# Optimization experiments

Hardware: AMD Instinct MI355X
Metric: run time of the kernel (lower is better)

The kernel has to match this reference:

```python
import jax, jax.numpy as jnp
import numpy as np

N = 65536
INPUT_DIM = 768
OUTPUT_DIM = 256
NUM_LEVELS = 4
CODEBOOK_SIZE = 1024
BETA = 0.25
LN_EPS = 1e-5


def setup_inputs() -> dict:
    key = jax.random.key(0)
    ks = jax.random.split(key, 12)
    s_in = 1.0 / np.sqrt(INPUT_DIM)
    s_out = 1.0 / np.sqrt(OUTPUT_DIM)
    return {
        "x": jax.random.normal(ks[0], (N, INPUT_DIM), dtype=jnp.float32),
        "ln_g": jnp.ones((INPUT_DIM,), dtype=jnp.float32),
        "ln_b": jnp.zeros((INPUT_DIM,), dtype=jnp.float32),
        # weights stored [in, out] (torch Linear is [out, in]); math identical
        "W1": jax.random.uniform(ks[1], (INPUT_DIM, OUTPUT_DIM), jnp.float32, -s_in, s_in),
        "b1": jax.random.uniform(ks[2], (OUTPUT_DIM,), jnp.float32, -s_in, s_in),
        "W2": jax.random.uniform(ks[3], (OUTPUT_DIM, OUTPUT_DIM), jnp.float32, -s_out, s_out),
        "b2": jax.random.uniform(ks[4], (OUTPUT_DIM,), jnp.float32, -s_out, s_out),
        "Wd1": jax.random.uniform(ks[5], (OUTPUT_DIM, INPUT_DIM), jnp.float32, -s_out, s_out),
        "bd1": jax.random.uniform(ks[6], (INPUT_DIM,), jnp.float32, -s_out, s_out),
        "Wd2": jax.random.uniform(ks[7], (INPUT_DIM, INPUT_DIM), jnp.float32, -s_in, s_in),
        "bd2": jax.random.uniform(ks[8], (INPUT_DIM,), jnp.float32, -s_in, s_in),
        "codebooks": jax.random.normal(ks[9], (NUM_LEVELS, CODEBOOK_SIZE, OUTPUT_DIM), dtype=jnp.float32),
    }


def _quantize_with_loss(enc, codebooks):
    residual = enc
    q_final = jnp.zeros_like(enc)
    commit = jnp.float32(0.0)
    indices = []
    for l in range(NUM_LEVELS):
        cb = codebooks[l]  # [K, D]
        # squared euclidean distance: ||r||^2 - 2 r.c + ||c||^2 -> [N, K]
        d = (jnp.sum(residual ** 2, axis=1, keepdims=True)
             - 2.0 * residual @ cb.T
             + jnp.sum(cb ** 2, axis=1)[None, :])
        idx = jnp.argmin(d, axis=1)  # [N]
        indices.append(idx)
        q = cb[idx]  # [N, D]
        commit = commit + jnp.mean((jax.lax.stop_gradient(residual) - q) ** 2)
        q_final = q_final + q
        q_st = residual + jax.lax.stop_gradient(q - residual)  # straight-through
        residual = residual - q_st
    return q_final, jnp.stack(indices, axis=1), commit


def reference(x, ln_g, ln_b, W1, b1, W2, b2, Wd1, bd1, Wd2, bd2, codebooks):
    # encoder: LayerNorm -> Linear -> ReLU -> Linear
    mu = jnp.mean(x, axis=-1, keepdims=True)
    var = jnp.mean((x - mu) ** 2, axis=-1, keepdims=True)
    xn = (x - mu) * jax.lax.rsqrt(var + LN_EPS) * ln_g + ln_b
    enc = jax.nn.relu(xn @ W1 + b1) @ W2 + b2  # [N, D]

    q, indices, commit = _quantize_with_loss(enc, codebooks)

    # decoder: Linear -> ReLU -> Linear
    recon = jax.nn.relu(q @ Wd1 + bd1) @ Wd2 + bd2  # [N, input_dim]

    rec_loss = jnp.mean((recon - x) ** 2)
    loss = rec_loss + BETA * commit
    return loss, recon, indices
```

## Files before the change

### kernel.cpp

```cpp
#include <hip/hip_runtime.h>
#include <hip/hip_bf16.h>
#include <stdint.h>

#define NROWS 65536
#define INDIM 768
#define ODIM  256
#define NLEV  4
#define CBS   1024
#define TAUQ  2e-2f

typedef __attribute__((ext_vector_type(8))) short short8;
typedef __attribute__((ext_vector_type(4))) float f32x4;

__device__ __forceinline__ float bf2f(unsigned short u) {
    union { unsigned int i; float f; } v; v.i = ((unsigned int)u) << 16; return v.f;
}
__device__ __forceinline__ unsigned short f2bf(float f) {
    union { float f; unsigned int i; } v; v.f = f;
    unsigned int r = v.i + 0x7fffu + ((v.i >> 16) & 1u);
    return (unsigned short)(r >> 16);
}
__device__ __forceinline__ f32x4 mfma_bf16(short8 a, short8 b, f32x4 c) {
    return __builtin_amdgcn_mfma_f32_16x16x32_bf16(a, b, c, 0, 0, 0);
}

typedef const __attribute__((address_space(1))) unsigned int GUI;
typedef __attribute__((address_space(3))) unsigned int LUI;
__device__ __forceinline__ void gld16(const void* g, void* l) {
    __builtin_amdgcn_global_load_lds((GUI*)g, (LUI*)l, 16, 0, 0);
}

__global__ void k_init(double* __restrict__ acc) {
    if (threadIdx.x < 2) acc[threadIdx.x] = 0.0;
}

__global__ __launch_bounds__(64) void k_cnorm(const float* __restrict__ cb, float* __restrict__ cn) {
    const int code = blockIdx.x;
    const float* r = cb + (size_t)code * ODIM + threadIdx.x * 4;
    float4 v = *(const float4*)r;
    float s = fmaf(v.x, v.x, fmaf(v.y, v.y, fmaf(v.z, v.z, v.w * v.w)));
    #pragma unroll
    for (int o = 32; o > 0; o >>= 1) s += __shfl_xor(s, o);
    if (threadIdx.x == 0) cn[code] = s;
}

__global__ __launch_bounds__(256) void k_split(const float* __restrict__ cb,
                                               unsigned short* __restrict__ ch,
                                               unsigned short* __restrict__ cl) {
    const size_t i = ((size_t)blockIdx.x * 256 + threadIdx.x) * 4;
    float4 v = *(const float4*)(cb + i);
    float e[4] = {v.x, v.y, v.z, v.w};
    ushort4 h, l;
    unsigned short* hp = &h.x; unsigned short* lp = &l.x;
    #pragma unroll
    for (int j = 0; j < 4; ++j) {
        unsigned short hh = f2bf(e[j]);
        hp[j] = hh;
        lp[j] = f2bf(e[j] - bf2f(hh));
    }
    *(ushort4*)(ch + i) = h;
    *(ushort4*)(cl + i) = l;
}

__global__ __launch_bounds__(256) void k_cbt(const float* __restrict__ cb, float* __restrict__ ct) {
    __shared__ float T[32][33];
    const int l  = blockIdx.z;
    const int c0 = blockIdx.x << 5;
    const int k0 = blockIdx.y << 5;
    const int tx = threadIdx.x & 31, ty = threadIdx.x >> 5;
    const float* src = cb + ((size_t)l * CBS + c0) * ODIM + k0;
    #pragma unroll
    for (int i = 0; i < 4; ++i)
        T[ty + (i << 3)][tx] = src[(size_t)(ty + (i << 3)) * ODIM + tx];
    __syncthreads();
    float* dst = ct + ((size_t)l * ODIM + k0) * CBS + c0;
    #pragma unroll
    for (int i = 0; i < 4; ++i)
        dst[(size_t)(ty + (i << 3)) * CBS + tx] = T[tx][ty + (i << 3)];
}

__global__ __launch_bounds__(256) void k_wt(const float* __restrict__ W,
                                            unsigned short* __restrict__ Th,
                                            unsigned short* __restrict__ Tl,
                                            const int K, const int N, const int split) {
    const int n = blockIdx.x;
    for (int k = threadIdx.x; k < K; k += 256) {
        float v = W[(size_t)k * N + n];
        unsigned short h = f2bf(v);
        Th[(size_t)n * K + k] = h;
        if (split) Tl[(size_t)n * K + k] = f2bf(v - bf2f(h));
    }
}

__global__ __launch_bounds__(256) void k_ln(const float* __restrict__ x,
                                            float* __restrict__ mu, float* __restrict__ rsig) {
    const int row = blockIdx.x;
    const int t = threadIdx.x;
    const float* xr = x + (size_t)row * INDIM;
    float a = xr[t], b = xr[t + 256], c = xr[t + 512];
    float s1 = a + b + c;
    float s2 = fmaf(a, a, fmaf(b, b, c * c));
    #pragma unroll
    for (int o = 32; o > 0; o >>= 1) { s1 += __shfl_xor(s1, o); s2 += __shfl_xor(s2, o); }
    __shared__ float r1[4], r2[4];
    if ((t & 63) == 0) { r1[t >> 6] = s1; r2[t >> 6] = s2; }
    __syncthreads();
    if (t == 0) {
        float S1 = (r1[0] + r1[1]) + (r1[2] + r1[3]);
        float S2 = (r2[0] + r2[1]) + (r2[2] + r2[3]);
        float m = S1 * (1.0f / INDIM);
        float var = S2 * (1.0f / INDIM) - m * m;
        mu[row] = m;
        rsig[row] = rsqrtf(var + 1e-5f);
    }
}

template <int AMODE, int SPLIT, int EPI>
__global__ __launch_bounds__(256, 2) void k_gemm_mfma(
    const void* __restrict__ Ap, const unsigned short* __restrict__ Bh,
    const unsigned short* __restrict__ Bl,
    const float* __restrict__ bias, void* __restrict__ Cp,
    const int K, const int Nc,
    const float* __restrict__ mu, const float* __restrict__ rsig,
    const float* __restrict__ lng, const float* __restrict__ lnb,
    const float* __restrict__ xref, double* __restrict__ acc_rec)
{
    __shared__ __align__(16) unsigned short BhS[256][40];
    __shared__ __align__(16) unsigned short BlS[SPLIT ? 256 : 8][SPLIT ? 40 : 8];
    __shared__ float credsh[4];

    const int t = threadIdx.x;
    const int wave = t >> 6, lane = t & 63;
    const int lg = lane >> 4, lm = lane & 15;
    const int wm = wave >> 1, wn = wave & 1;
    const size_t rowb = (size_t)blockIdx.y * 128 + wm * 64;
    const int nb = blockIdx.x << 8;

    f32x4 acc[4][8];
    #pragma unroll
    for (int mt = 0; mt < 4; ++mt)
        #pragma unroll
        for (int nt = 0; nt < 8; ++nt) acc[mt][nt] = (f32x4){0.f, 0.f, 0.f, 0.f};

    float lnm[4], lnr[4];
    if (AMODE == 1) {
        #pragma unroll
        for (int mt = 0; mt < 4; ++mt) {
            lnm[mt] = mu[rowb + (mt << 4) + lm];
            lnr[mt] = rsig[rowb + (mt << 4) + lm];
        }
    }

    for (int kk = 0; kk < K; kk += 32) {
        short8 Ah[4], Al[4];
        if (AMODE == 2) {
            #pragma unroll
            for (int mt = 0; mt < 4; ++mt)
                Ah[mt] = *(const short8*)((const unsigned short*)Ap +
                          (rowb + (mt << 4) + lm) * (size_t)K + kk + (lg << 3));
        } else {
            float g[8], bb[8];
            if (AMODE == 1) {
                float4 g0 = *(const float4*)(lng + kk + (lg << 3));
                float4 g1 = *(const float4*)(lng + kk + (lg << 3) + 4);
                float4 b0 = *(const float4*)(lnb + kk + (lg << 3));
                float4 b1 = *(const float4*)(lnb + kk + (lg << 3) + 4);
                g[0]=g0.x; g[1]=g0.y; g[2]=g0.z; g[3]=g0.w; g[4]=g1.x; g[5]=g1.y; g[6]=g1.z; g[7]=g1.w;
                bb[0]=b0.x; bb[1]=b0.y; bb[2]=b0.z; bb[3]=b0.w; bb[4]=b1.x; bb[5]=b1.y; bb[6]=b1.z; bb[7]=b1.w;
            }
            #pragma unroll
            for (int mt = 0; mt < 4; ++mt) {
                const float* ar = (const float*)Ap + (rowb + (mt << 4) + lm) * (size_t)K + kk + (lg << 3);
                float4 a0 = *(const float4*)ar;
                float4 a1 = *(const float4*)(ar + 4);
                float e[8] = {a0.x, a0.y, a0.z, a0.w, a1.x, a1.y, a1.z, a1.w};
                #pragma unroll
                for (int j = 0; j < 8; ++j) {
                    float v = e[j];
                    if (AMODE == 1) v = fmaf((v - lnm[mt]) * lnr[mt], g[j], bb[j]);
                    unsigned short h = f2bf(v);
                    Ah[mt][j] = (short)h;
                    Al[mt][j] = (short)f2bf(v - bf2f(h));
                }
            }
        }
        __syncthreads();
        {
            const unsigned short* gh = Bh + (size_t)nb * K + kk;
            #pragma unroll
            for (int it = 0; it < 4; ++it) {
                const int idx = (it << 8) + t;
                const int n = idx >> 2, sl = idx & 3;
                *(uint4*)&BhS[n][sl << 3] = *(const uint4*)(gh + (size_t)n * K + (sl << 3));
            }
            if (SPLIT) {
                const unsigned short* gl = Bl + (size_t)nb * K + kk;
                #pragma unroll
                for (int it = 0; it < 4; ++it) {
                    const int idx = (it << 8) + t;
                    const int n = idx >> 2, sl = idx & 3;
                    *(uint4*)&BlS[n][sl << 3] = *(const uint4*)(gl + (size_t)n * K + (sl << 3));
                }
            }
        }
        __syncthreads();
        #pragma unroll
        for (int nt = 0; nt < 8; ++nt) {
            const int nl = (wn << 7) + (nt << 4) + lm;
            short8 bh = *(const short8*)&BhS[nl][lg << 3];
            if (!SPLIT) {
                #pragma unroll
                for (int mt = 0; mt < 4; ++mt)
                    acc[mt][nt] = mfma_bf16(Ah[mt], bh, acc[mt][nt]);
            } else {
                short8 bl = *(const short8*)&BlS[nl][lg << 3];
                #pragma unroll
                for (int mt = 0; mt < 4; ++mt) {
                    acc[mt][nt] = mfma_bf16(Ah[mt], bh, acc[mt][nt]);
                    acc[mt][nt] = mfma_bf16(Al[mt], bh, acc[mt][nt]);
                    acc[mt][nt] = mfma_bf16(Ah[mt], bl, acc[mt][nt]);
                }
            }
        }
    }

    float lsum = 0.0f;
    #pragma unroll
    for (int nt = 0; nt < 8; ++nt) {
        const int col = nb + (wn << 7) + (nt << 4) + lm;
        const float bs = bias[col];
        #pragma unroll
        for (int mt = 0; mt < 4; ++mt) {
            #pragma unroll
            for (int r = 0; r < 4; ++r) {
                float v = acc[mt][nt][r] + bs;
                if (EPI == 0 || EPI == 2) v = fmaxf(v, 0.0f);
                const size_t row = rowb + (mt << 4) + (lg << 2) + r;
                if (EPI == 2) {
                    ((unsigned short*)Cp)[row * Nc + col] = f2bf(v);
                } else {
                    ((float*)Cp)[row * Nc + col] = v;
                }
                if (EPI == 3) {
                    const float d = v - xref[row * Nc + col];
                    lsum = fmaf(d, d, lsum);
                }
            }
        }
    }
    if (EPI == 3) {
        #pragma unroll
        for (int o = 32; o > 0; o >>= 1) lsum += __shfl_xor(lsum, o);
        if (lane == 0) credsh[wave] = lsum;
        __syncthreads();
        if (t == 0) atomicAdd(acc_rec, (double)((credsh[0] + credsh[1]) + (credsh[2] + credsh[3])));
    }
}

__global__ __launch_bounds__(256, 2) void k_quant_mfma(
    const float* __restrict__ enc, const float* __restrict__ cb,
    const unsigned short* __restrict__ cbh, const unsigned short* __restrict__ cbl,
    const float* __restrict__ cnorm, unsigned short* __restrict__ qf, float* __restrict__ oidx,
    int* __restrict__ flag, double* __restrict__ acc_commit)
{
    __shared__ __align__(128) unsigned short Bh[2][32][256];
    __shared__ __align__(128) unsigned short Bl[2][32][256];
    __shared__ __align__(16) int rowidxsh[128];
    __shared__ float credsh[4];

    const int t = threadIdx.x;
    const int wave = t >> 6, lane = t & 63;
    const int lg = lane >> 4, lm = lane & 15;
    const size_t rowbase = (size_t)blockIdx.x * 128 + wave * 32;

#define STAGE_CHUNK(b_, gh_, gl_) do {                                          \
    _Pragma("unroll")                                                           \
    for (int i_ = 0; i_ < 4; ++i_) {                                            \
        const int seg_ = (i_ << 2) + wave;                                      \
        const int off_ = (seg_ << 10) + (lane << 4);                            \
        const int src_ = off_ ^ (((off_ >> 9) & 7) << 4);                       \
        gld16((const char*)(gh_) + src_, (char*)&Bh[b_][0][0] + (seg_ << 10));  \
        gld16((const char*)(gl_) + src_, (char*)&Bl[b_][0][0] + (seg_ << 10));  \
    }                                                                           \
} while (0)

    STAGE_CHUNK(0, cbh, cbl);
    int buf = 0;

    short8 Ah[2][8], Al[2][8];
    #pragma unroll
    for (int mt = 0; mt < 2; ++mt)
        #pragma unroll
        for (int s = 0; s < 8; ++s) {
            const float* er = enc + (rowbase + mt * 16 + lm) * ODIM + s * 32 + lg * 8;
            float4 e0 = *(const float4*)er;
            float4 e1 = *(const float4*)(er + 4);
            float e[8] = {e0.x, e0.y, e0.z, e0.w, e1.x, e1.y, e1.z, e1.w};
            #pragma unroll
            for (int j = 0; j < 8; ++j) {
                unsigned short h = f2bf(e[j]);
                Ah[mt][s][j] = (short)h;
                Al[mt][s][j] = (short)f2bf(e[j] - bf2f(h));
            }
        }

    float commit_local = 0.0f;
    int flg[2][4] = {{0, 0, 0, 0}, {0, 0, 0, 0}};

    for (int l = 0; l < NLEV; ++l) {
        float bestv[2][4], b2v[2][4];
        int besti[2][4];
        #pragma unroll
        for (int mt = 0; mt < 2; ++mt)
            #pragma unroll
            for (int r = 0; r < 4; ++r) { bestv[mt][r] = 3.4e38f; b2v[mt][r] = 3.4e38f; besti[mt][r] = 0; }

        for (int ch = 0; ch < 32; ++ch) {
            __syncthreads();
            {
                const int cc = (l << 5) + ch + 1;
                if (cc < 128) {
                    const unsigned short* gh = cbh + ((size_t)(cc >> 5) << 18) + ((size_t)(cc & 31) << 13);
                    const unsigned short* gl = cbl + ((size_t)(cc >> 5) << 18) + ((size_t)(cc & 31) << 13);
                    STAGE_CHUNK(buf ^ 1, gh, gl);
                }
            }
            const int cbase = ch << 5;
            const unsigned short* bbh = &Bh[buf][0][0];
            const unsigned short* bbl = &Bl[buf][0][0];
            #pragma unroll
            for (int nt = 0; nt < 2; ++nt) {
                const int rowB = (nt << 4) + lm;
                const int rbase = rowB << 9;
                const int xm = (rowB & 7) << 4;
                f32x4 p0[2], p1[2];
                #pragma unroll
                for (int mt = 0; mt < 2; ++mt) {
                    p0[mt] = (f32x4){0.f, 0.f, 0.f, 0.f};
                    p1[mt] = (f32x4){0.f, 0.f, 0.f, 0.f};
                }
                #pragma unroll
                for (int s = 0; s < 8; ++s) {
                    const int a = rbase + (((s << 6) + (lg << 4)) ^ xm);
                    short8 bh = *(const short8*)((const char*)bbh + a);
                    short8 bl = *(const short8*)((const char*)bbl + a);
                    p0[0] = mfma_bf16(Ah[0][s], bh, p0[0]);
                    p0[1] = mfma_bf16(Ah[1][s], bh, p0[1]);
                    p1[0] = mfma_bf16(Al[0][s], bh, p1[0]);
                    p1[1] = mfma_bf16(Al[1][s], bh, p1[1]);
                    p1[0] = mfma_bf16(Ah[0][s], bl, p1[0]);
                    p1[1] = mfma_bf16(Ah[1][s], bl, p1[1]);
                }
                const int code = cbase + (nt << 4) + lm;
                const float cn = cnorm[(l << 10) + code];
                #pragma unroll
                for (int mt = 0; mt < 2; ++mt)
                    #pragma unroll
                    for (int r = 0; r < 4; ++r) {
                        const float d = fmaf(-2.0f, p0[mt][r] + p1[mt][r], cn);
                        if (d < bestv[mt][r]) {
                            b2v[mt][r] = bestv[mt][r]; bestv[mt][r] = d; besti[mt][r] = code;
                        } else {
                            b2v[mt][r] = fminf(b2v[mt][r], d);
                        }
                    }
            }
            buf ^= 1;
        }

        #pragma unroll
        for (int mt = 0; mt < 2; ++mt) {
            int iv[4];
            #pragma unroll
            for (int r = 0; r < 4; ++r) {
                float bv = bestv[mt][r], b2 = b2v[mt][r];
                int bi = besti[mt][r];
                #pragma unroll
                for (int off = 1; off < 16; off <<= 1) {
                    float ov = __shfl_xor(bv, off);
                    float o2 = __shfl_xor(b2, off);
                    int   oi = __shfl_xor(bi, off);
                    if (ov < bv)      { b2 = fminf(bv, o2); bv = ov; bi = oi; }
                    else if (ov > bv) { b2 = fminf(b2, ov); }
                    else              { b2 = bv; bi = (oi < bi) ? oi : bi; }
                }
                flg[mt][r] |= (b2 - bv < TAUQ) ? 1 : 0;
                iv[r] = bi;
                if (lm == 0)
                    oidx[(rowbase + (mt << 4) + (lg << 2) + r) * NLEV + l] = (float)bi;
            }
            if (lm == 0)
                *(int4*)&rowidxsh[(wave << 5) + (mt << 4) + (lg << 2)] = make_int4(iv[0], iv[1], iv[2], iv[3]);
        }
        __syncthreads();

        const size_t lbase = (size_t)l * CBS * ODIM;
        #pragma unroll
        for (int mt = 0; mt < 2; ++mt) {
            const int ci = rowidxsh[(wave << 5) + (mt << 4) + lm];
            const float* cr = cb + lbase + (size_t)ci * ODIM + lg * 8;
            #pragma unroll
            for (int s = 0; s < 8; ++s) {
                float4 c0 = *(const float4*)(cr + (s << 5));
                float4 c1 = *(const float4*)(cr + (s << 5) + 4);
                float c[8] = {c0.x, c0.y, c0.z, c0.w, c1.x, c1.y, c1.z, c1.w};
                #pragma unroll
                for (int j = 0; j < 8; ++j) {
                    float rr = bf2f((unsigned short)Ah[mt][s][j]) + bf2f((unsigned short)Al[mt][s][j]) - c[j];
                    commit_local = fmaf(rr, rr, commit_local);
                    unsigned short h = f2bf(rr);
                    Ah[mt][s][j] = (short)h;
                    Al[mt][s][j] = (short)f2bf(rr - bf2f(h));
                }
            }
        }
    }
#undef STAGE_CHUNK

    #pragma unroll
    for (int mt = 0; mt < 2; ++mt)
        #pragma unroll
        for (int s = 0; s < 8; ++s) {
            const size_t ro = (rowbase + mt * 16 + lm) * ODIM + s * 32 + lg * 8;
            float4 e0 = *(const float4*)(enc + ro);
            float4 e1 = *(const float4*)(enc + ro + 4);
            float e[8] = {e0.x, e0.y, e0.z, e0.w, e1.x, e1.y, e1.z, e1.w};
            unsigned short q[8];
            #pragma unroll
            for (int j = 0; j < 8; ++j)
                q[j] = f2bf(e[j] - (bf2f((unsigned short)Ah[mt][s][j]) + bf2f((unsigned short)Al[mt][s][j])));
            *(ushort4*)(qf + ro)     = make_ushort4(q[0], q[1], q[2], q[3]);
            *(ushort4*)(qf + ro + 4) = make_ushort4(q[4], q[5], q[6], q[7]);
        }

    if (lm == 0) {
        #pragma unroll
        for (int mt = 0; mt < 2; ++mt)
            #pragma unroll
            for (int r = 0; r < 4; ++r)
                flag[rowbase + (mt << 4) + (lg << 2) + r] = flg[mt][r];
    }

    #pragma unroll
    for (int o = 32; o > 0; o >>= 1) commit_local += __shfl_xor(commit_local, o);
    if (lane == 0) credsh[wave] = commit_local;
    __syncthreads();
    if (t == 0) atomicAdd(acc_commit, (double)((credsh[0] + credsh[1]) + (credsh[2] + credsh[3])));
}

__global__ __launch_bounds__(256) void k_fix(
    const int* __restrict__ flag, const float* __restrict__ x,
    const float* __restrict__ lng, const float* __restrict__ lnb,
    const float* __restrict__ W1, const float* __restrict__ b1,
    const float* __restrict__ W2, const float* __restrict__ b2,
    const float* __restrict__ cb, const float* __restrict__ ct,
    float* __restrict__ oidx)
{
    const int row = blockIdx.x;
    if (!flag[row]) return;
    const int t = threadIdx.x;
    __shared__ double xn[INDIM];
    __shared__ double hs[ODIM];
    __shared__ double r[ODIM];
    __shared__ double rv_[4];
    __shared__ int ri_[4];
    __shared__ int selidx;

    const float* xr = x + (size_t)row * INDIM;
    double xa = (double)xr[t], xb = (double)xr[t + 256], xc = (double)xr[t + 512];
    double s1 = xa + xb + xc;
    double s2 = xa * xa + xb * xb + xc * xc;
    #pragma unroll
    for (int o = 32; o > 0; o >>= 1) { s1 += __shfl_xor(s1, o); s2 += __shfl_xor(s2, o); }
    __shared__ double w1r[4], w2r[4];
    if ((t & 63) == 0) { w1r[t >> 6] = s1; w2r[t >> 6] = s2; }
    __syncthreads();
    double S1 = (w1r[0] + w1r[1]) + (w1r[2] + w1r[3]);
    double S2 = (w2r[0] + w2r[1]) + (w2r[2] + w2r[3]);
    double mu = S1 / (double)INDIM;
    double var = S2 / (double)INDIM - mu * mu;
    double rs = 1.0 / sqrt(var + 1e-5);
    xn[t]       = (xa - mu) * rs * (double)lng[t]       + (double)lnb[t];
    xn[t + 256] = (xb - mu) * rs * (double)lng[t + 256] + (double)lnb[t + 256];
    xn[t + 512] = (xc - mu) * rs * (double)lng[t + 512] + (double)lnb[t + 512];
    __syncthreads();
    {
        double a0 = 0.0, a1 = 0.0, a2 = 0.0, a3 = 0.0;
        for (int k = 0; k < INDIM; k += 4) {
            a0 = fma(xn[k + 0], (double)W1[(size_t)(k + 0) * ODIM + t], a0);
            a1 = fma(xn[k + 1], (double)W1[(size_t)(k + 1) * ODIM + t], a1);
            a2 = fma(xn[k + 2], (double)W1[(size_t)(k + 2) * ODIM + t], a2);
            a3 = fma(xn[k + 3], (double)W1[(size_t)(k + 3) * ODIM + t], a3);
        }
        hs[t] = fmax(((a0 + a1) + (a2 + a3)) + (double)b1[t], 0.0);
    }
    __syncthreads();
    {
        double a0 = 0.0, a1 = 0.0, a2 = 0.0, a3 = 0.0;
        for (int k = 0; k < ODIM; k += 4) {
            a0 = fma(hs[k + 0], (double)W2[(size_t)(k + 0) * ODIM + t], a0);
            a1 = fma(hs[k + 1], (double)W2[(size_t)(k + 1) * ODIM + t], a1);
            a2 = fma(hs[k + 2], (double)W2[(size_t)(k + 2) * ODIM + t], a2);
            a3 = fma(hs[k + 3], (double)W2[(size_t)(k + 3) * ODIM + t], a3);
        }
        r[t] = ((a0 + a1) + (a2 + a3)) + (double)b2[t];
    }
    __syncthreads();

    for (int l = 0; l < NLEV; ++l) {
        const float* ctl = ct + (size_t)l * CBS * ODIM;
        double d0 = 0.0, d1 = 0.0, d2 = 0.0, d3 = 0.0;
        #pragma unroll 4
        for (int k = 0; k < ODIM; ++k) {
            const double rk = r[k];
            const float4 c4 = *(const float4*)(ctl + ((size_t)k << 10) + (t << 2));
            const double f0 = rk - (double)c4.x;
            const double f1 = rk - (double)c4.y;
            const double f2 = rk - (double)c4.z;
            const double f3 = rk - (double)c4.w;
            d0 = fma(f0, f0, d0); d1 = fma(f1, f1, d1);
            d2 = fma(f2, f2, d2); d3 = fma(f3, f3, d3);
        }
        double bv = d0; int bi = (t << 2);
        if (d1 < bv) { bv = d1; bi = (t << 2) + 1; }
        if (d2 < bv) { bv = d2; bi = (t << 2) + 2; }
        if (d3 < bv) { bv = d3; bi = (t << 2) + 3; }
        #pragma unroll
        for (int o = 32; o > 0; o >>= 1) {
            double ov = __shfl_xor(bv, o);
            int oi = __shfl_xor(bi, o);
            if (ov < bv || (ov == bv && oi < bi)) { bv = ov; bi = oi; }
        }
        if ((t & 63) == 0) { rv_[t >> 6] = bv; ri_[t >> 6] = bi; }
        __syncthreads();
        if (t == 0) {
            double fv = rv_[0]; int fi = ri_[0];
            #pragma unroll
            for (int w = 1; w < 4; ++w)
                if (rv_[w] < fv || (rv_[w] == fv && ri_[w] < fi)) { fv = rv_[w]; fi = ri_[w]; }
            selidx = fi;
            oidx[(size_t)row * NLEV + l] = (float)fi;
        }
        __syncthreads();
        r[t] = r[t] - (double)cb[(size_t)l * CBS * ODIM + (size_t)selidx * ODIM + t];
        __syncthreads();
    }
}

__global__ void k_fin(const double* __restrict__ acc, float* __restrict__ out) {
    if (threadIdx.x == 0)
        out[0] = (float)(acc[1] / ((double)NROWS * (double)INDIM) +
                         0.25 * (acc[0] / ((double)NROWS * (double)ODIM)));
}

extern "C" void kernel_launch(void* const* d_in, const int* in_sizes, int n_in,
                              void* d_out, int out_size, void* d_ws, size_t ws_size,
                              hipStream_t stream)
{
    const float* x   = (const float*)d_in[0];
    const float* lng = (const float*)d_in[1];
    const float* lnb = (const float*)d_in[2];
    const float* W1  = (const float*)d_in[3];
    const float* b1  = (const float*)d_in[4];
    const float* W2  = (const float*)d_in[5];
    const float* b2  = (const float*)d_in[6];
    const float* Wd1 = (const float*)d_in[7];
    const float* bd1 = (const float*)d_in[8];
    const float* Wd2 = (const float*)d_in[9];
    const float* bd2 = (const float*)d_in[10];
    const float* cbs = (const float*)d_in[11];

    char* ws = (char*)d_ws;
    const size_t MB = 1u << 20;
    const size_t O_ACC  = 0;
    const size_t O_CN   = 1024;
    const size_t O_MU   = O_CN + 16384;
    const size_t O_RS   = O_MU + (size_t)NROWS * 4;
    const size_t O_FLAG = O_RS + (size_t)NROWS * 4;
    const size_t O_ENC  = 1 * MB;
    const size_t O_QF   = 65 * MB;
    const size_t O_W1H  = 97 * MB;
    const size_t O_W1L  = O_W1H + (size_t)INDIM * ODIM * 2;
    const size_t O_W2H  = O_W1L + (size_t)INDIM * ODIM * 2;
    const size_t O_W2L  = O_W2H + (size_t)ODIM * ODIM * 2;
    const size_t O_WD1  = O_W2L + (size_t)ODIM * ODIM * 2;
    const size_t O_WD2  = O_WD1 + (size_t)ODIM * INDIM * 2;
    const size_t O_CBH  = 100 * MB;
    const size_t O_CBL  = 102 * MB;
    const size_t O_H1   = 104 * MB;
    const size_t O_CT   = O_H1;

    double* acc   = (double*)(ws + O_ACC);
    float* cnorm  = (float*)(ws + O_CN);
    float* mu     = (float*)(ws + O_MU);
    float* rsig   = (float*)(ws + O_RS);
    int*   flag   = (int*)(ws + O_FLAG);
    float* enc    = (float*)(ws + O_ENC);
    unsigned short* qf  = (unsigned short*)(ws + O_QF);
    unsigned short* w1h = (unsigned short*)(ws + O_W1H);
    unsigned short* w1l = (unsigned short*)(ws + O_W1L);
    unsigned short* w2h = (unsigned short*)(ws + O_W2H);
    unsigned short* w2l = (unsigned short*)(ws + O_W2L);
    unsigned short* wd1h = (unsigned short*)(ws + O_WD1);
    unsigned short* wd2h = (unsigned short*)(ws + O_WD2);
    unsigned short* cbh = (unsigned short*)(ws + O_CBH);
    unsigned short* cbl = (unsigned short*)(ws + O_CBL);
    float* h1     = (float*)(ws + O_H1);
    float* ct     = (float*)(ws + O_CT);
    unsigned short* hd = (unsigned short*)(ws + O_H1);

    float* outF  = (float*)d_out;
    float* recon = outF + 1;
    float* oidx  = outF + 1 + (size_t)NROWS * INDIM;

    k_init<<<1, 64, 0, stream>>>(acc);
    k_cnorm<<<NLEV * CBS, 64, 0, stream>>>(cbs, cnorm);
    k_ln<<<NROWS, 256, 0, stream>>>(x, mu, rsig);
    k_wt<<<ODIM, 256, 0, stream>>>(W1, w1h, w1l, INDIM, ODIM, 1);
    k_wt<<<ODIM, 256, 0, stream>>>(W2, w2h, w2l, ODIM, ODIM, 1);
    k_wt<<<INDIM, 256, 0, stream>>>(Wd1, wd1h, nullptr, ODIM, INDIM, 0);
    k_wt<<<INDIM, 256, 0, stream>>>(Wd2, wd2h, nullptr, INDIM, INDIM, 0);
    k_split<<<(NLEV * CBS * ODIM) / 1024, 256, 0, stream>>>(cbs, cbh, cbl);
    k_gemm_mfma<1, 1, 0><<<dim3(1, NROWS / 128), 256, 0, stream>>>(
        x, w1h, w1l, b1, h1, INDIM, ODIM, mu, rsig, lng, lnb, nullptr, nullptr);
    k_gemm_mfma<0, 1, 1><<<dim3(1, NROWS / 128), 256, 0, stream>>>(
        h1, w2h, w2l, b2, enc, ODIM, ODIM, nullptr, nullptr, nullptr, nullptr, nullptr, nullptr);
    k_cbt<<<dim3(32, 8, 4), 256, 0, stream>>>(cbs, ct);
    k_quant_mfma<<<NROWS / 128, 256, 0, stream>>>(enc, cbs, cbh, cbl, cnorm, qf, oidx, flag, acc);
    k_fix<<<NROWS, 256, 0, stream>>>(flag, x, lng, lnb, W1, b1, W2, b2, cbs, ct, oidx);
    k_gemm_mfma<2, 0, 2><<<dim3(INDIM / 256, NROWS / 128), 256, 0, stream>>>(
        qf, wd1h, nullptr, bd1, hd, ODIM, INDIM, nullptr, nullptr, nullptr, nullptr, nullptr, nullptr);
    k_gemm_mfma<2, 0, 3><<<dim3(INDIM / 256, NROWS / 128), 256, 0, stream>>>(
        hd, wd2h, nullptr, bd2, recon, INDIM, INDIM, nullptr, nullptr, nullptr, nullptr, x, acc + 1);
    k_fin<<<1, 64, 0, stream>>>(acc, outF);
}
```

Before: 1.626 ms.

## Shrink quantizer tile to 16 rows per wave with single-buffered padded LDS

Reworks the residual quantization kernel so each wave handles 16 rows instead of 32 and blocks cover 64 rows, doubling the grid and raising the occupancy target. The asynchronous double-buffered direct-to-LDS codebook staging with XOR swizzle is replaced by synchronous register-staged loads into a padded LDS tile, bracketed by two barriers per chunk. This aims to cut register pressure and raise occupancy, at the cost of halving codebook reuse per LDS load, doubling total codebook reads, and losing load/compute overlap.

```diff
diff --git a/kernel.cpp b/kernel.cpp
--- a/kernel.cpp
+++ b/kernel.cpp
@@ -22,12 +22,6 @@
 }
 __device__ __forceinline__ f32x4 mfma_bf16(short8 a, short8 b, f32x4 c) {
     return __builtin_amdgcn_mfma_f32_16x16x32_bf16(a, b, c, 0, 0, 0);
-}
-
-typedef const __attribute__((address_space(1))) unsigned int GUI;
-typedef __attribute__((address_space(3))) unsigned int LUI;
-__device__ __forceinline__ void gld16(const void* g, void* l) {
-    __builtin_amdgcn_global_load_lds((GUI*)g, (LUI*)l, 16, 0, 0);
 }
 
 __global__ void k_init(double* __restrict__ acc) {
@@ -257,124 +251,101 @@
     }
 }
 
-__global__ __launch_bounds__(256, 2) void k_quant_mfma(
+__global__ __launch_bounds__(256, 4) void k_quant_mfma(
     const float* __restrict__ enc, const float* __restrict__ cb,
     const unsigned short* __restrict__ cbh, const unsigned short* __restrict__ cbl,
     const float* __restrict__ cnorm, unsigned short* __restrict__ qf, float* __restrict__ oidx,
     int* __restrict__ flag, double* __restrict__ acc_commit)
 {
-    __shared__ __align__(128) unsigned short Bh[2][32][256];
-    __shared__ __align__(128) unsigned short Bl[2][32][256];
-    __shared__ __align__(16) int rowidxsh[128];
+    __shared__ __align__(16) unsigned short Bh[32][264];
+    __shared__ __align__(16) unsigned short Bl[32][264];
+    __shared__ __align__(16) int rowidxsh[64];
     __shared__ float credsh[4];
 
     const int t = threadIdx.x;
     const int wave = t >> 6, lane = t & 63;
     const int lg = lane >> 4, lm = lane & 15;
-    const size_t rowbase = (size_t)blockIdx.x * 128 + wave * 32;
-
-#define STAGE_CHUNK(b_, gh_, gl_) do {                                          \
-    _Pragma("unroll")                                                           \
-    for (int i_ = 0; i_ < 4; ++i_) {                                            \
-        const int seg_ = (i_ << 2) + wave;                                      \
-        const int off_ = (seg_ << 10) + (lane << 4);                            \
-        const int src_ = off_ ^ (((off_ >> 9) & 7) << 4);                       \
-        gld16((const char*)(gh_) + src_, (char*)&Bh[b_][0][0] + (seg_ << 10));  \
-        gld16((const char*)(gl_) + src_, (char*)&Bl[b_][0][0] + (seg_ << 10));  \
-    }                                                                           \
-} while (0)
-
-    STAGE_CHUNK(0, cbh, cbl);
-    int buf = 0;
-
-    short8 Ah[2][8], Al[2][8];
-    #pragma unroll
-    for (int mt = 0; mt < 2; ++mt)
-        #pragma unroll
-        for (int s = 0; s < 8; ++s) {
-            const float* er = enc + (rowbase + mt * 16 + lm) * ODIM + s * 32 + lg * 8;
-            float4 e0 = *(const float4*)er;
-            float4 e1 = *(const float4*)(er + 4);
-            float e[8] = {e0.x, e0.y, e0.z, e0.w, e1.x, e1.y, e1.z, e1.w};
-            #pragma unroll
-            for (int j = 0; j < 8; ++j) {
-                unsigned short h = f2bf(e[j]);
-                Ah[mt][s][j] = (short)h;
-                Al[mt][s][j] = (short)f2bf(e[j] - bf2f(h));
-            }
-        }
+    const size_t rowbase = (size_t)blockIdx.x * 64 + wave * 16;
+
+    short8 Ah[8], Al[8];
+    #pragma unroll
+    for (int s = 0; s < 8; ++s) {
+        const float* er = enc + (rowbase + lm) * ODIM + s * 32 + lg * 8;
+        float4 e0 = *(const float4*)er;
+        float4 e1 = *(const float4*)(er + 4);
+        float e[8] = {e0.x, e0.y, e0.z, e0.w, e1.x, e1.y, e1.z, e1.w};
+        #pragma unroll
+        for (int j = 0; j < 8; ++j) {
+            unsigned short h = f2bf(e[j]);
+            Ah[s][j] = (short)h;
+            Al[s][j] = (short)f2bf(e[j] - bf2f(h));
+        }
+    }
 
     float commit_local = 0.0f;
-    int flg[2][4] = {{0, 0, 0, 0}, {0, 0, 0, 0}};
+    int flg[4] = {0, 0, 0, 0};
 
     for (int l = 0; l < NLEV; ++l) {
-        float bestv[2][4], b2v[2][4];
-        int besti[2][4];
-        #pragma unroll
-        for (int mt = 0; mt < 2; ++mt)
-            #pragma unroll
-            for (int r = 0; r < 4; ++r) { bestv[mt][r] = 3.4e38f; b2v[mt][r] = 3.4e38f; besti[mt][r] = 0; }
+        const size_t lbase = (size_t)l * CBS * ODIM;
+        float bestv[4], b2v[4];
+        int besti[4];
+        #pragma unroll
+        for (int r = 0; r < 4; ++r) { bestv[r] = 3.4e38f; b2v[r] = 3.4e38f; besti[r] = 0; }
 
         for (int ch = 0; ch < 32; ++ch) {
+            const int cbase = ch << 5;
             __syncthreads();
             {
-                const int cc = (l << 5) + ch + 1;
-                if (cc < 128) {
-                    const unsigned short* gh = cbh + ((size_t)(cc >> 5) << 18) + ((size_t)(cc & 31) << 13);
-                    const unsigned short* gl = cbl + ((size_t)(cc >> 5) << 18) + ((size_t)(cc & 31) << 13);
-                    STAGE_CHUNK(buf ^ 1, gh, gl);
-                }
-            }
-            const int cbase = ch << 5;
-            const unsigned short* bbh = &Bh[buf][0][0];
-            const unsigned short* bbl = &Bl[buf][0][0];
+                const unsigned short* gh = cbh + lbase + (size_t)cbase * ODIM;
+                const unsigned short* gl = cbl + lbase + (size_t)cbase * ODIM;
+                #pragma unroll
+                for (int r = 0; r < 4; ++r) {
+                    const int i = (r << 8) + t;
+                    const int code = i >> 5, sl = i & 31;
+                    *(uint4*)&Bh[code][sl << 3] = *(const uint4*)(gh + ((size_t)i << 3));
+                    *(uint4*)&Bl[code][sl << 3] = *(const uint4*)(gl + ((size_t)i << 3));
+                }
+            }
+            __syncthreads();
+            f32x4 p0[2], p1[2];
             #pragma unroll
             for (int nt = 0; nt < 2; ++nt) {
-                const int rowB = (nt << 4) + lm;
-                const int rbase = rowB << 9;
-                const int xm = (rowB & 7) << 4;
-                f32x4 p0[2], p1[2];
-                #pragma unroll
-                for (int mt = 0; mt < 2; ++mt) {
-                    p0[mt] = (f32x4){0.f, 0.f, 0.f, 0.f};
-                    p1[mt] = (f32x4){0.f, 0.f, 0.f, 0.f};
-                }
-                #pragma unroll
-                for (int s = 0; s < 8; ++s) {
-                    const int a = rbase + (((s << 6) + (lg << 4)) ^ xm);
-                    short8 bh = *(const short8*)((const char*)bbh + a);
-                    short8 bl = *(const short8*)((const char*)bbl + a);
-                    p0[0] = mfma_bf16(Ah[0][s], bh, p0[0]);
-                    p0[1] = mfma_bf16(Ah[1][s], bh, p0[1]);
-                    p1[0] = mfma_bf16(Al[0][s], bh, p1[0]);
-                    p1[1] = mfma_bf16(Al[1][s], bh, p1[1]);
-                    p1[0] = mfma_bf16(Ah[0][s], bl, p1[0]);
-                    p1[1] = mfma_bf16(Ah[1][s], bl, p1[1]);
-                }
+                p0[nt] = (f32x4){0.f, 0.f, 0.f, 0.f};
+                p1[nt] = (f32x4){0.f, 0.f, 0.f, 0.f};
+            }
+            #pragma unroll
+            for (int s = 0; s < 8; ++s) {
+                #pragma unroll
+                for (int nt = 0; nt < 2; ++nt) {
+                    short8 bh = *(const short8*)&Bh[(nt << 4) + lm][(s << 5) + (lg << 3)];
+                    short8 bl = *(const short8*)&Bl[(nt << 4) + lm][(s << 5) + (lg << 3)];
+                    p0[nt] = mfma_bf16(Ah[s], bh, p0[nt]);
+                    p1[nt] = mfma_bf16(Al[s], bh, p1[nt]);
+                    p1[nt] = mfma_bf16(Ah[s], bl, p1[nt]);
+                }
+            }
+            #pragma unroll
+            for (int nt = 0; nt < 2; ++nt) {
                 const int code = cbase + (nt << 4) + lm;
                 const float cn = cnorm[(l << 10) + code];
                 #pragma unroll
-                for (int mt = 0; mt < 2; ++mt)
-                    #pragma unroll
-                    for (int r = 0; r < 4; ++r) {
-                        const float d = fmaf(-2.0f, p0[mt][r] + p1[mt][r], cn);
-                        if (d < bestv[mt][r]) {
-                            b2v[mt][r] = bestv[mt][r]; bestv[mt][r] = d; besti[mt][r] = code;
-                        } else {
-                            b2v[mt][r] = fminf(b2v[mt][r], d);
-                        }
+                for (int r = 0; r < 4; ++r) {
+                    const float d = fmaf(-2.0f, p0[nt][r] + p1[nt][r], cn);
+                    if (d < bestv[r]) {
+                        b2v[r] = bestv[r]; bestv[r] = d; besti[r] = code;
+                    } else {
+                        b2v[r] = fminf(b2v[r], d);
                     }
-            }
-            buf ^= 1;
-        }
-
-        #pragma unroll
-        for (int mt = 0; mt < 2; ++mt) {
+                }
+            }
+        }
+
+        {
             int iv[4];
             #pragma unroll
             for (int r = 0; r < 4; ++r) {
-                float bv = bestv[mt][r], b2 = b2v[mt][r];
-                int bi = besti[mt][r];
+                float bv = bestv[r], b2 = b2v[r];
+                int bi = besti[r];
                 #pragma unroll
                 for (int off = 1; off < 16; off <<= 1) {
                     float ov = __shfl_xor(bv, off);
@@ -384,20 +355,18 @@
                     else if (ov > bv) { b2 = fminf(b2, ov); }
                     else              { b2 = bv; bi = (oi < bi) ? oi : bi; }
                 }
-                flg[mt][r] |= (b2 - bv < TAUQ) ? 1 : 0;
+                flg[r] |= (b2 - bv < TAUQ) ? 1 : 0;
                 iv[r] = bi;
                 if (lm == 0)
-                    oidx[(rowbase + (mt << 4) + (lg << 2) + r) * NLEV + l] = (float)bi;
+                    oidx[(rowbase + (lg << 2) + r) * NLEV + l] = (float)bi;
             }
             if (lm == 0)
-                *(int4*)&rowidxsh[(wave << 5) + (mt << 4) + (lg << 2)] = make_int4(iv[0], iv[1], iv[2], iv[3]);
+                *(int4*)&rowidxsh[(wave << 4) + (lg << 2)] = make_int4(iv[0], iv[1], iv[2], iv[3]);
         }
         __syncthreads();
 
-        const size_t lbase = (size_t)l * CBS * ODIM;
-        #pragma unroll
-        for (int mt = 0; mt < 2; ++mt) {
-            const int ci = rowidxsh[(wave << 5) + (mt << 4) + lm];
+        {
+            const int ci = rowidxsh[(wave << 4) + lm];
             const float* cr = cb + lbase + (size_t)ci * ODIM + lg * 8;
             #pragma unroll
             for (int s = 0; s < 8; ++s) {
@@ -406,39 +375,34 @@
                 float c[8] = {c0.x, c0.y, c0.z, c0.w, c1.x, c1.y, c1.z, c1.w};
                 #pragma unroll
                 for (int j = 0; j < 8; ++j) {
-                    float rr = bf2f((unsigned short)Ah[mt][s][j]) + bf2f((unsigned short)Al[mt][s][j]) - c[j];
+                    float rr = bf2f((unsigned short)Ah[s][j]) + bf2f((unsigned short)Al[s][j]) - c[j];
                     commit_local = fmaf(rr, rr, commit_local);
                     unsigned short h = f2bf(rr);
-                    Ah[mt][s][j] = (short)h;
-                    Al[mt][s][j] = (short)f2bf(rr - bf2f(h));
-                }
-            }
-        }
-    }
-#undef STAGE_CHUNK
-
-    #pragma unroll
-    for (int mt = 0; mt < 2; ++mt)
-        #pragma unroll
-        for (int s = 0; s < 8; ++s) {
-            const size_t ro = (rowbase + mt * 16 + lm) * ODIM + s * 32 + lg * 8;
-            float4 e0 = *(const float4*)(enc + ro);
-            float4 e1 = *(const float4*)(enc + ro + 4);
-            float e[8] = {e0.x, e0.y, e0.z, e0.w, e1.x, e1.y, e1.z, e1.w};
-            unsigned short q[8];
-            #pragma unroll
-            for (int j = 0; j < 8; ++j)
-                q[j] = f2bf(e[j] - (bf2f((unsigned short)Ah[mt][s][j]) + bf2f((unsigned short)Al[mt][s][j])));
-            *(ushort4*)(qf + ro)     = make_ushort4(q[0], q[1], q[2], q[3]);
-            *(ushort4*)(qf + ro + 4) = make_ushort4(q[4], q[5], q[6], q[7]);
-        }
+                    Ah[s][j] = (short)h;
+                    Al[s][j] = (short)f2bf(rr - bf2f(h));
+                }
+            }
+        }
+    }
+
+    #pragma unroll
+    for (int s = 0; s < 8; ++s) {
+        const size_t ro = (rowbase + lm) * ODIM + s * 32 + lg * 8;
+        float4 e0 = *(const float4*)(enc + ro);
+        float4 e1 = *(const float4*)(enc + ro + 4);
+        float e[8] = {e0.x, e0.y, e0.z, e0.w, e1.x, e1.y, e1.z, e1.w};
+        unsigned short q[8];
+        #pragma unroll
+        for (int j = 0; j < 8; ++j)
+            q[j] = f2bf(e[j] - (bf2f((unsigned short)Ah[s][j]) + bf2f((unsigned short)Al[s][j])));
+        *(ushort4*)(qf + ro)     = make_ushort4(q[0], q[1], q[2], q[3]);
+        *(ushort4*)(qf + ro + 4) = make_ushort4(q[4], q[5], q[6], q[7]);
+    }
 
     if (lm == 0) {
         #pragma unroll
-        for (int mt = 0; mt < 2; ++mt)
-            #pragma unroll
-            for (int r = 0; r < 4; ++r)
-                flag[rowbase + (mt << 4) + (lg << 2) + r] = flg[mt][r];
+        for (int r = 0; r < 4; ++r)
+            flag[rowbase + (lg << 2) + r] = flg[r];
     }
 
     #pragma unroll
@@ -626,7 +590,7 @@
     k_gemm_mfma<0, 1, 1><<<dim3(1, NROWS / 128), 256, 0, stream>>>(
         h1, w2h, w2l, b2, enc, ODIM, ODIM, nullptr, nullptr, nullptr, nullptr, nullptr, nullptr);
     k_cbt<<<dim3(32, 8, 4), 256, 0, stream>>>(cbs, ct);
-    k_quant_mfma<<<NROWS / 128, 256, 0, stream>>>(enc, cbs, cbh, cbl, cnorm, qf, oidx, flag, acc);
+    k_quant_mfma<<<NROWS / 64, 256, 0, stream>>>(enc, cbs, cbh, cbl, cnorm, qf, oidx, flag, acc);
     k_fix<<<NROWS, 256, 0, stream>>>(flag, x, lng, lnb, W1, b1, W2, b2, cbs, ct, oidx);
     k_gemm_mfma<2, 0, 2><<<dim3(INDIM / 256, NROWS / 128), 256, 0, stream>>>(
         qf, wd1h, nullptr, bd1, hd, ODIM, INDIM, nullptr, nullptr, nullptr, nullptr, nullptr, nullptr);
```

Measured after the change: 2.002 ms. 23.1% more time.

## Replace async double-buffered codebook staging with synchronous padded LDS in quantizer

Applied to the files above, without the earlier changes.

The quantizer kernel drops the global_load_lds double-buffered prefetch with XOR swizzle. It now copies each codebook chunk through registers into a single padded LDS buffer, with a barrier before compute. Blocks shrink from 256 to 128 threads (64 rows each), and all MFMAs for both code tiles are issued before the distance epilogue. Each block re-reads the codebook while covering fewer rows, and load latency is no longer overlapped with compute, in exchange for more blocks and simpler addressing.

```diff
diff --git a/kernel.cpp b/kernel.cpp
--- a/kernel.cpp
+++ b/kernel.cpp
@@ -22,12 +22,6 @@
 }
 __device__ __forceinline__ f32x4 mfma_bf16(short8 a, short8 b, f32x4 c) {
     return __builtin_amdgcn_mfma_f32_16x16x32_bf16(a, b, c, 0, 0, 0);
-}
-
-typedef const __attribute__((address_space(1))) unsigned int GUI;
-typedef __attribute__((address_space(3))) unsigned int LUI;
-__device__ __forceinline__ void gld16(const void* g, void* l) {
-    __builtin_amdgcn_global_load_lds((GUI*)g, (LUI*)l, 16, 0, 0);
 }
 
 __global__ void k_init(double* __restrict__ acc) {
@@ -257,35 +251,21 @@
     }
 }
 
-__global__ __launch_bounds__(256, 2) void k_quant_mfma(
+__global__ __launch_bounds__(128, 2) void k_quant_mfma(
     const float* __restrict__ enc, const float* __restrict__ cb,
     const unsigned short* __restrict__ cbh, const unsigned short* __restrict__ cbl,
     const float* __restrict__ cnorm, unsigned short* __restrict__ qf, float* __restrict__ oidx,
     int* __restrict__ flag, double* __restrict__ acc_commit)
 {
-    __shared__ __align__(128) unsigned short Bh[2][32][256];
-    __shared__ __align__(128) unsigned short Bl[2][32][256];
-    __shared__ __align__(16) int rowidxsh[128];
-    __shared__ float credsh[4];
+    __shared__ __align__(16) unsigned short Bh[32][264];
+    __shared__ __align__(16) unsigned short Bl[32][264];
+    __shared__ __align__(16) int rowidxsh[64];
+    __shared__ float credsh[2];
 
     const int t = threadIdx.x;
     const int wave = t >> 6, lane = t & 63;
     const int lg = lane >> 4, lm = lane & 15;
-    const size_t rowbase = (size_t)blockIdx.x * 128 + wave * 32;
-
-#define STAGE_CHUNK(b_, gh_, gl_) do {                                          \
-    _Pragma("unroll")                                                           \
-    for (int i_ = 0; i_ < 4; ++i_) {                                            \
-        const int seg_ = (i_ << 2) + wave;                                      \
-        const int off_ = (seg_ << 10) + (lane << 4);                            \
-        const int src_ = off_ ^ (((off_ >> 9) & 7) << 4);                       \
-        gld16((const char*)(gh_) + src_, (char*)&Bh[b_][0][0] + (seg_ << 10));  \
-        gld16((const char*)(gl_) + src_, (char*)&Bl[b_][0][0] + (seg_ << 10));  \
-    }                                                                           \
-} while (0)
-
-    STAGE_CHUNK(0, cbh, cbl);
-    int buf = 0;
+    const size_t rowbase = (size_t)blockIdx.x * 64 + wave * 32;
 
     short8 Ah[2][8], Al[2][8];
     #pragma unroll
@@ -308,6 +288,7 @@
     int flg[2][4] = {{0, 0, 0, 0}, {0, 0, 0, 0}};
 
     for (int l = 0; l < NLEV; ++l) {
+        const size_t lbase = (size_t)l * CBS * ODIM;
         float bestv[2][4], b2v[2][4];
         int besti[2][4];
         #pragma unroll
@@ -316,48 +297,51 @@
             for (int r = 0; r < 4; ++r) { bestv[mt][r] = 3.4e38f; b2v[mt][r] = 3.4e38f; besti[mt][r] = 0; }
 
         for (int ch = 0; ch < 32; ++ch) {
+            const int cbase = ch << 5;
             __syncthreads();
             {
-                const int cc = (l << 5) + ch + 1;
-                if (cc < 128) {
-                    const unsigned short* gh = cbh + ((size_t)(cc >> 5) << 18) + ((size_t)(cc & 31) << 13);
-                    const unsigned short* gl = cbl + ((size_t)(cc >> 5) << 18) + ((size_t)(cc & 31) << 13);
-                    STAGE_CHUNK(buf ^ 1, gh, gl);
-                }
-            }
-            const int cbase = ch << 5;
-            const unsigned short* bbh = &Bh[buf][0][0];
-            const unsigned short* bbl = &Bl[buf][0][0];
+                const unsigned short* gh = cbh + lbase + (size_t)cbase * ODIM;
+                const unsigned short* gl = cbl + lbase + (size_t)cbase * ODIM;
+                #pragma unroll
+                for (int r = 0; r < 8; ++r) {
+                    const int i = (r << 7) + t;
+                    const int code = i >> 5, sl = i & 31;
+                    *(uint4*)&Bh[code][sl << 3] = *(const uint4*)(gh + ((size_t)i << 3));
+                    *(uint4*)&Bl[code][sl << 3] = *(const uint4*)(gl + ((size_t)i << 3));
+                }
+            }
+            __syncthreads();
+            f32x4 p0[2][2], p1[2][2];
+            #pragma unroll
+            for (int mt = 0; mt < 2; ++mt)
+                #pragma unroll
+                for (int nt = 0; nt < 2; ++nt) {
+                    p0[mt][nt] = (f32x4){0.f, 0.f, 0.f, 0.f};
+                    p1[mt][nt] = (f32x4){0.f, 0.f, 0.f, 0.f};
+                }
+            #pragma unroll
+            for (int s = 0; s < 8; ++s) {
+                #pragma unroll
+                for (int nt = 0; nt < 2; ++nt) {
+                    short8 bh = *(const short8*)&Bh[(nt << 4) + lm][(s << 5) + (lg << 3)];
+                    short8 bl = *(const short8*)&Bl[(nt << 4) + lm][(s << 5) + (lg << 3)];
+                    p0[0][nt] = mfma_bf16(Ah[0][s], bh, p0[0][nt]);
+                    p0[1][nt] = mfma_bf16(Ah[1][s], bh, p0[1][nt]);
+                    p1[0][nt] = mfma_bf16(Al[0][s], bh, p1[0][nt]);
+                    p1[1][nt] = mfma_bf16(Al[1][s], bh, p1[1][nt]);
+                    p1[0][nt] = mfma_bf16(Ah[0][s], bl, p1[0][nt]);
+                    p1[1][nt] = mfma_bf16(Ah[1][s], bl, p1[1][nt]);
+                }
+            }
             #pragma unroll
             for (int nt = 0; nt < 2; ++nt) {
-                const int rowB = (nt << 4) + lm;
-                const int rbase = rowB << 9;
-                const int xm = (rowB & 7) << 4;
-                f32x4 p0[2], p1[2];
-                #pragma unroll
-                for (int mt = 0; mt < 2; ++mt) {
-                    p0[mt] = (f32x4){0.f, 0.f, 0.f, 0.f};
-                    p1[mt] = (f32x4){0.f, 0.f, 0.f, 0.f};
-                }
-                #pragma unroll
-                for (int s = 0; s < 8; ++s) {
-                    const int a = rbase + (((s << 6) + (lg << 4)) ^ xm);
-                    short8 bh = *(const short8*)((const char*)bbh + a);
-                    short8 bl = *(const short8*)((const char*)bbl + a);
-                    p0[0] = mfma_bf16(Ah[0][s], bh, p0[0]);
-                    p0[1] = mfma_bf16(Ah[1][s], bh, p0[1]);
-                    p1[0] = mfma_bf16(Al[0][s], bh, p1[0]);
-                    p1[1] = mfma_bf16(Al[1][s], bh, p1[1]);
-                    p1[0] = mfma_bf16(Ah[0][s], bl, p1[0]);
-                    p1[1] = mfma_bf16(Ah[1][s], bl, p1[1]);
-                }
                 const int code = cbase + (nt << 4) + lm;
                 const float cn = cnorm[(l << 10) + code];
                 #pragma unroll
                 for (int mt = 0; mt < 2; ++mt)
                     #pragma unroll
                     for (int r = 0; r < 4; ++r) {
-                        const float d = fmaf(-2.0f, p0[mt][r] + p1[mt][r], cn);
+                        const float d = fmaf(-2.0f, p0[mt][nt][r] + p1[mt][nt][r], cn);
                         if (d < bestv[mt][r]) {
                             b2v[mt][r] = bestv[mt][r]; bestv[mt][r] = d; besti[mt][r] = code;
                         } else {
@@ -365,7 +349,6 @@
                         }
                     }
             }
-            buf ^= 1;
         }
 
         #pragma unroll
@@ -394,7 +377,6 @@
         }
         __syncthreads();
 
-        const size_t lbase = (size_t)l * CBS * ODIM;
         #pragma unroll
         for (int mt = 0; mt < 2; ++mt) {
             const int ci = rowidxsh[(wave << 5) + (mt << 4) + lm];
@@ -415,7 +397,6 @@
             }
         }
     }
-#undef STAGE_CHUNK
 
     #pragma unroll
     for (int mt = 0; mt < 2; ++mt)
@@ -445,7 +426,7 @@
     for (int o = 32; o > 0; o >>= 1) commit_local += __shfl_xor(commit_local, o);
     if (lane == 0) credsh[wave] = commit_local;
     __syncthreads();
-    if (t == 0) atomicAdd(acc_commit, (double)((credsh[0] + credsh[1]) + (credsh[2] + credsh[3])));
+    if (t == 0) atomicAdd(acc_commit, (double)(credsh[0] + credsh[1]));
 }
 
 __global__ __launch_bounds__(256) void k_fix(
@@ -626,7 +607,7 @@
     k_gemm_mfma<0, 1, 1><<<dim3(1, NROWS / 128), 256, 0, stream>>>(
         h1, w2h, w2l, b2, enc, ODIM, ODIM, nullptr, nullptr, nullptr, nullptr, nullptr, nullptr);
     k_cbt<<<dim3(32, 8, 4), 256, 0, stream>>>(cbs, ct);
-    k_quant_mfma<<<NROWS / 128, 256, 0, stream>>>(enc, cbs, cbh, cbl, cnorm, qf, oidx, flag, acc);
+    k_quant_mfma<<<NROWS / 64, 128, 0, stream>>>(enc, cbs, cbh, cbl, cnorm, qf, oidx, flag, acc);
     k_fix<<<NROWS, 256, 0, stream>>>(flag, x, lng, lnb, W1, b1, W2, b2, cbs, ct, oidx);
     k_gemm_mfma<2, 0, 2><<<dim3(INDIM / 256, NROWS / 128), 256, 0, stream>>>(
         qf, wd1h, nullptr, bd1, hd, ODIM, INDIM, nullptr, nullptr, nullptr, nullptr, nullptr, nullptr);
```

Result: slower. 2.443 ms (+50.2%).
